# Optimization experiments

Hardware: AMD Instinct MI355X
Metric: run time of the kernel (lower is better)

Reference implementation:

```python
import jax, jax.numpy as jnp
import numpy as np

N = 8192      # nodes
D_IN = 128    # input features
D_H = 48      # GAT hidden (hardcoded in module)
D_OUT = 32    # control output dim
NEG_INF = -9e15  # matches torch code's -9000000000000000.0


def setup_inputs() -> dict:
    key = jax.random.key(0)
    ks = jax.random.split(key, 12)
    s = 0.05
    return {
        "x": jax.random.normal(ks[0], (N, D_IN), jnp.float32),
        "adj": jax.random.randint(ks[1], (N, N), 0, 2, jnp.int32),
        "W_gat": jax.random.normal(ks[2], (D_H, D_IN), jnp.float32) * s,
        "a": jax.random.normal(ks[3], (1, D_H), jnp.float32) * s,
        "gamma": jnp.ones((D_H,), jnp.float32),
        "beta": jnp.zeros((D_H,), jnp.float32),
        "W1": jax.random.normal(ks[4], (256, D_H), jnp.float32) * s,
        "b1": jnp.zeros((256,), jnp.float32),
        "W2": jax.random.normal(ks[5], (128, 256), jnp.float32) * s,
        "b2": jnp.zeros((128,), jnp.float32),
        "W3": jax.random.normal(ks[6], (D_OUT, 128), jnp.float32) * s,
        "b3": jnp.zeros((D_OUT,), jnp.float32),
    }


def reference(x, adj, W_gat, a, gamma, beta, W1, b1, W2, b2, W3, b3):
    # --- LightweightGATLayer ---
    Wh = x @ W_gat.T                      # [N, D_H]
    s = Wh @ a.T                          # [N, 1] additive attention scores
    e = s + s.T                           # [N, N]
    e = jnp.where(e > 0, e, 0.2 * e)      # LeakyReLU(0.2)
    e = jnp.where(adj > 0, e, NEG_INF)    # mask non-edges
    attn = jax.nn.softmax(e, axis=1)      # row softmax; dropout is identity in eval
    h_prime = attn @ Wh                   # [N, D_H]
    # LayerNorm over last dim, eps=1e-5
    mu = jnp.mean(h_prime, axis=-1, keepdims=True)
    var = jnp.var(h_prime, axis=-1, keepdims=True)
    h = (h_prime - mu) * jax.lax.rsqrt(var + 1e-5) * gamma + beta
    # --- BiACT MLP head: 48 -> 256 -> 128 -> D_OUT ---
    h = jax.nn.relu(h @ W1.T + b1)
    h = jax.nn.relu(h @ W2.T + b2)
    return h @ W3.T + b3                  # [N, D_OUT]
```

## Files before the change

### kernel.cpp

```cpp
#include <hip/hip_runtime.h>

#define N 8192
#define DIN 128
#define DH 48
#define MT 256
#define KC 64
#define PSTR (KC + 8)
#define NSPLIT 16
#define JSPAN (N / NSPLIT)
#define NCHUNK (JSPAN / KC)
#define ACC_STRIDE 64
#define RB 32

typedef _Float16 half8 __attribute__((ext_vector_type(8)));
typedef float f32x4 __attribute__((ext_vector_type(4)));

__global__ __launch_bounds__(256) void k_wh(const float* __restrict__ x,
                                            const float* __restrict__ Wg,
                                            float* __restrict__ Wh) {
    __shared__ float wT[DIN * DH];
    int t = threadIdx.x;
    for (int e = t; e < DIN * DH; e += 256) {
        int c = e / DIN, k = e % DIN;
        wT[k * DH + c] = Wg[e];
    }
    __syncthreads();
    int o = blockIdx.x * 256 + t;
    int r = o / DH, c = o % DH;
    const float4* xr = (const float4*)(x + (size_t)r * DIN);
    float acc = 0.f;
    #pragma unroll 8
    for (int k4 = 0; k4 < DIN / 4; ++k4) {
        float4 xv = xr[k4];
        int kb = k4 * 4;
        acc += xv.x * wT[(kb + 0) * DH + c];
        acc += xv.y * wT[(kb + 1) * DH + c];
        acc += xv.z * wT[(kb + 2) * DH + c];
        acc += xv.w * wT[(kb + 3) * DH + c];
    }
    Wh[o] = acc;
}

__global__ __launch_bounds__(256) void k_s(const float* __restrict__ Wh,
                                           const float* __restrict__ a,
                                           float* __restrict__ s) {
    int r = blockIdx.x * 256 + threadIdx.x;
    const float4* wr = (const float4*)(Wh + (size_t)r * DH);
    const float4* av = (const float4*)a;
    float acc = 0.f;
    #pragma unroll
    for (int k4 = 0; k4 < DH / 4; ++k4) {
        float4 w = wr[k4]; float4 aa = av[k4];
        acc += w.x * aa.x + w.y * aa.y + w.z * aa.z + w.w * aa.w;
    }
    s[r] = acc;
}

__global__ __launch_bounds__(256) void k_gat(const int* __restrict__ adj,
                                             const float* __restrict__ Wh,
                                             const float* __restrict__ s,
                                             float* __restrict__ accWs) {
    __shared__ _Float16 pS[MT][PSTR];
    __shared__ _Float16 wS[64][PSTR];
    __shared__ float sRow[MT];
    int t = threadIdx.x;
    int tile = blockIdx.x & 31;
    int split = blockIdx.x >> 5;
    int i0 = tile * MT;
    int jbase = split * JSPAN;

    sRow[t] = s[i0 + t];
    for (int e = t; e < 16 * PSTR; e += 256) {
        int n = 48 + e / PSTR, k = e % PSTR;
        wS[n][k] = (n == 48) ? (_Float16)1.0f : (_Float16)0.0f;
    }

    int lane = t & 63, w = t >> 6;
    int ln16 = lane & 15, kq = lane >> 4;
    int jp = t & 31, rg = t >> 5;

    f32x4 acc[4][4];
    #pragma unroll
    for (int a0 = 0; a0 < 4; ++a0)
        #pragma unroll
        for (int b0 = 0; b0 < 4; ++b0) acc[a0][b0] = (f32x4){0.f, 0.f, 0.f, 0.f};

    __syncthreads();

    for (int chunk = 0; chunk < NCHUNK; ++chunk) {
        int j0 = jbase + chunk * KC;
        #pragma unroll
        for (int k = 0; k < 12; ++k) {
            int e = t + k * 256;
            int jc = e / DH, d = e % DH;
            wS[d][jc] = (_Float16)Wh[(size_t)j0 * DH + e];
        }
        {
            float2 sj = *(const float2*)(s + j0 + 2 * jp);
            #pragma unroll 8
            for (int it = 0; it < 32; ++it) {
                int r = rg * 32 + it;
                int2 av = *(const int2*)(adj + (size_t)(i0 + r) * N + j0 + 2 * jp);
                float e0 = sRow[r] + sj.x;
                float e1 = sRow[r] + sj.y;
                e0 = fmaxf(e0, 0.2f * e0);
                e1 = fmaxf(e1, 0.2f * e1);
                float p0 = av.x ? __expf(e0) : 0.f;
                float p1 = av.y ? __expf(e1) : 0.f;
                union { _Float16 h[2]; unsigned u; } pk;
                pk.h[0] = (_Float16)p0;
                pk.h[1] = (_Float16)p1;
                *(unsigned*)&pS[r][2 * jp] = pk.u;
            }
        }
        __syncthreads();
        {
            const int m0 = w * 64;
            #pragma unroll
            for (int kt = 0; kt < 2; ++kt) {
                const int kk = kt * 32 + kq * 8;
                half8 b[4];
                #pragma unroll
                for (int nt = 0; nt < 4; ++nt)
                    b[nt] = *(const half8*)&wS[nt * 16 + ln16][kk];
                #pragma unroll
                for (int mtl = 0; mtl < 4; ++mtl) {
                    half8 a = *(const half8*)&pS[m0 + mtl * 16 + ln16][kk];
                    #pragma unroll
                    for (int nt = 0; nt < 4; ++nt)
                        acc[mtl][nt] = __builtin_amdgcn_mfma_f32_16x16x32_f16(
                            a, b[nt], acc[mtl][nt], 0, 0, 0);
                }
            }
        }
        __syncthreads();
    }
    size_t rbase = (size_t)split * N + i0;
    #pragma unroll
    for (int mtl = 0; mtl < 4; ++mtl) {
        #pragma unroll
        for (int nt = 0; nt < 4; ++nt) {
            int col = nt * 16 + ln16;
            if (nt == 3 && ln16 != 0) continue;
            #pragma unroll
            for (int reg = 0; reg < 4; ++reg) {
                int row = w * 64 + mtl * 16 + kq * 4 + reg;
                accWs[(rbase + row) * ACC_STRIDE + col] = acc[mtl][nt][reg];
            }
        }
    }
}

__global__ __launch_bounds__(256) void k_mlp(const float* __restrict__ accWs,
                                             const float* __restrict__ gamma,
                                             const float* __restrict__ beta,
                                             const float* __restrict__ W1, const float* __restrict__ b1,
                                             const float* __restrict__ W2, const float* __restrict__ b2,
                                             const float* __restrict__ W3, const float* __restrict__ b3,
                                             float* __restrict__ out) {
    __shared__ float hacc[RB * 49];
    __shared__ float hN[RB * DH];
    __shared__ float h1[RB * 256];
    __shared__ float h2[RB * 128];
    int t = threadIdx.x;
    int r0 = blockIdx.x * RB;

    for (int e = t; e < RB * 49; e += 256) {
        int r = e / 49, d = e % 49;
        size_t base = (size_t)(r0 + r) * ACC_STRIDE + d;
        float v = 0.f;
        #pragma unroll
        for (int sp = 0; sp < NSPLIT; ++sp)
            v += accWs[(size_t)sp * N * ACC_STRIDE + base];
        hacc[r * 49 + d] = v;
    }
    __syncthreads();

    if (t < RB) {
        float invl = 1.f / hacc[t * 49 + 48];
        float sum = 0.f;
        for (int d = 0; d < DH; ++d) sum += hacc[t * 49 + d];
        float mean = sum * invl * (1.f / DH);
        float var = 0.f;
        for (int d = 0; d < DH; ++d) {
            float dv = hacc[t * 49 + d] * invl - mean;
            var += dv * dv;
        }
        var *= (1.f / DH);
        float rs = rsqrtf(var + 1e-5f);
        for (int d = 0; d < DH; ++d) {
            float hv = (hacc[t * 49 + d] * invl - mean) * rs;
            hN[t * DH + d] = hv * gamma[d] + beta[d];
        }
    }
    __syncthreads();

    {
        int c = t;
        float4 wreg[12];
        const float4* wrow = (const float4*)(W1 + c * DH);
        #pragma unroll
        for (int k4 = 0; k4 < 12; ++k4) wreg[k4] = wrow[k4];
        float bias = b1[c];
        for (int r = 0; r < RB; ++r) {
            float acc = bias;
            const float4* hv4 = (const float4*)&hN[r * DH];
            #pragma unroll
            for (int k4 = 0; k4 < 12; ++k4) {
                float4 hv = hv4[k4];
                acc += hv.x * wreg[k4].x + hv.y * wreg[k4].y
                     + hv.z * wreg[k4].z + hv.w * wreg[k4].w;
            }
            h1[r * 256 + c] = fmaxf(acc, 0.f);
        }
    }
    __syncthreads();

    {
        int c = t & 127;
        int g = t >> 7;
        int rb = g * 16;
        float acc[16];
        float bias = b2[c];
        #pragma unroll
        for (int r = 0; r < 16; ++r) acc[r] = bias;
        const float4* wrow = (const float4*)(W2 + c * 256);
        for (int k4 = 0; k4 < 64; ++k4) {
            float4 wv = wrow[k4];
            #pragma unroll
            for (int r = 0; r < 16; ++r) {
                const float4 hv = *(const float4*)(&h1[(rb + r) * 256 + k4 * 4]);
                acc[r] += wv.x * hv.x + wv.y * hv.y + wv.z * hv.z + wv.w * hv.w;
            }
        }
        #pragma unroll
        for (int r = 0; r < 16; ++r)
            h2[(rb + r) * 128 + c] = fmaxf(acc[r], 0.f);
    }
    __syncthreads();

    {
        int c = t & 31;
        int g = t >> 5;
        int rb = g * 4;
        float acc[4];
        float bias = b3[c];
        #pragma unroll
        for (int r = 0; r < 4; ++r) acc[r] = bias;
        const float4* wrow = (const float4*)(W3 + c * 128);
        for (int k4 = 0; k4 < 32; ++k4) {
            float4 wv = wrow[k4];
            #pragma unroll
            for (int r = 0; r < 4; ++r) {
                const float4 hv = *(const float4*)(&h2[(rb + r) * 128 + k4 * 4]);
                acc[r] += wv.x * hv.x + wv.y * hv.y + wv.z * hv.z + wv.w * hv.w;
            }
        }
        #pragma unroll
        for (int r = 0; r < 4; ++r)
            out[(size_t)(r0 + rb + r) * 32 + c] = acc[r];
    }
}

extern "C" void kernel_launch(void* const* d_in, const int* in_sizes, int n_in,
                              void* d_out, int out_size, void* d_ws, size_t ws_size,
                              hipStream_t stream) {
    const float* x     = (const float*)d_in[0];
    const int*   adj   = (const int*)d_in[1];
    const float* Wg    = (const float*)d_in[2];
    const float* a     = (const float*)d_in[3];
    const float* gamma = (const float*)d_in[4];
    const float* beta  = (const float*)d_in[5];
    const float* W1    = (const float*)d_in[6];
    const float* b1    = (const float*)d_in[7];
    const float* W2    = (const float*)d_in[8];
    const float* b2    = (const float*)d_in[9];
    const float* W3    = (const float*)d_in[10];
    const float* b3    = (const float*)d_in[11];
    float* out = (float*)d_out;

    float* ws = (float*)d_ws;
    float* Wh    = ws;
    float* s     = ws + (size_t)N * DH;
    float* accWs = s + N;

    k_wh<<<N * DH / 256, 256, 0, stream>>>(x, Wg, Wh);
    k_s<<<N / 256, 256, 0, stream>>>(Wh, a, s);
    k_gat<<<32 * NSPLIT, 256, 0, stream>>>(adj, Wh, s, accWs);
    k_mlp<<<N / RB, 256, 0, stream>>>(accWs, gamma, beta, W1, b1, W2, b2, W3, b3, out);
}
```

Baseline: 463.4 us.

## Halve GAT tile, pre-transpose Wh to fp16, atomically reduce splits, retile MLP

The GAT row tile shrinks from 256 to 128 rows, which doubles the grid, and the kernel sets launch bounds for higher occupancy. Wh is pre-transposed to fp16 in a separate kernel so B fragments load straight from global memory instead of being staged through LDS. The denominator column now comes from a constant register fragment, and the adjacency loads for a chunk are batched up front. The 16 split partials are combined with atomicAdd into a zeroed buffer rather than written out and summed in the MLP. The MLP layers 1 and 2 are also retiled for more register reuse. In exchange this adds extra launches, atomic traffic and re-reads of adjacency-independent data per tile.

```diff
diff --git a/kernel.cpp b/kernel.cpp
--- a/kernel.cpp
+++ b/kernel.cpp
@@ -3,17 +3,22 @@
 #define N 8192
 #define DIN 128
 #define DH 48
-#define MT 256
+#define MT 128
 #define KC 64
-#define PSTR (KC + 8)
+#define PSTR 72
 #define NSPLIT 16
 #define JSPAN (N / NSPLIT)
 #define NCHUNK (JSPAN / KC)
-#define ACC_STRIDE 64
+#define HSTR 49
 #define RB 32
 
 typedef _Float16 half8 __attribute__((ext_vector_type(8)));
 typedef float f32x4 __attribute__((ext_vector_type(4)));
+
+__global__ __launch_bounds__(256) void k_zero(float* __restrict__ hacc) {
+    int i = blockIdx.x * 256 + threadIdx.x;
+    if (i < N * HSTR) hacc[i] = 0.f;
+}
 
 __global__ __launch_bounds__(256) void k_wh(const float* __restrict__ x,
                                             const float* __restrict__ Wg,
@@ -56,57 +61,82 @@
     s[r] = acc;
 }
 
-__global__ __launch_bounds__(256) void k_gat(const int* __restrict__ adj,
-                                             const float* __restrict__ Wh,
-                                             const float* __restrict__ s,
-                                             float* __restrict__ accWs) {
+__global__ __launch_bounds__(256) void k_tr(const float* __restrict__ Wh,
+                                            _Float16* __restrict__ WhT) {
+    __shared__ _Float16 tile[DH][72];
+    int t = threadIdx.x;
+    int r0 = blockIdx.x * 64;
+    for (int e = t; e < 64 * DH; e += 256) {
+        int r = e / DH, c = e % DH;
+        tile[c][r] = (_Float16)Wh[(size_t)(r0 + r) * DH + c];
+    }
+    __syncthreads();
+    for (int u = t; u < DH * 8; u += 256) {
+        int c = u >> 3, g = u & 7;
+        *(half8*)&WhT[(size_t)c * N + r0 + g * 8] = *(const half8*)&tile[c][g * 8];
+    }
+}
+
+__global__ __launch_bounds__(256, 4) void k_gat(const int* __restrict__ adj,
+                                                const _Float16* __restrict__ WhT,
+                                                const float* __restrict__ s,
+                                                float* __restrict__ hacc) {
     __shared__ _Float16 pS[MT][PSTR];
-    __shared__ _Float16 wS[64][PSTR];
     __shared__ float sRow[MT];
     int t = threadIdx.x;
-    int tile = blockIdx.x & 31;
-    int split = blockIdx.x >> 5;
+    int tile = blockIdx.x & 63;
+    int split = blockIdx.x >> 6;
     int i0 = tile * MT;
     int jbase = split * JSPAN;
 
-    sRow[t] = s[i0 + t];
-    for (int e = t; e < 16 * PSTR; e += 256) {
-        int n = 48 + e / PSTR, k = e % PSTR;
-        wS[n][k] = (n == 48) ? (_Float16)1.0f : (_Float16)0.0f;
-    }
+    if (t < MT) sRow[t] = s[i0 + t];
 
     int lane = t & 63, w = t >> 6;
     int ln16 = lane & 15, kq = lane >> 4;
     int jp = t & 31, rg = t >> 5;
 
-    f32x4 acc[4][4];
+    half8 bc;
+    {
+        _Float16 v = (ln16 == 0) ? (_Float16)1.0f : (_Float16)0.0f;
+        #pragma unroll
+        for (int i = 0; i < 8; ++i) bc[i] = v;
+    }
+
+    f32x4 acc[2][4];
     #pragma unroll
-    for (int a0 = 0; a0 < 4; ++a0)
-        #pragma unroll
-        for (int b0 = 0; b0 < 4; ++b0) acc[a0][b0] = (f32x4){0.f, 0.f, 0.f, 0.f};
+    for (int m = 0; m < 2; ++m)
+        #pragma unroll
+        for (int n = 0; n < 4; ++n) acc[m][n] = (f32x4){0.f, 0.f, 0.f, 0.f};
 
     __syncthreads();
 
     for (int chunk = 0; chunk < NCHUNK; ++chunk) {
         int j0 = jbase + chunk * KC;
-        #pragma unroll
-        for (int k = 0; k < 12; ++k) {
-            int e = t + k * 256;
-            int jc = e / DH, d = e % DH;
-            wS[d][jc] = (_Float16)Wh[(size_t)j0 * DH + e];
-        }
+        int2 av[16];
+        {
+            const int* abase = adj + (size_t)(i0 + rg * 16) * N + j0 + 2 * jp;
+            #pragma unroll
+            for (int it = 0; it < 16; ++it)
+                av[it] = *(const int2*)(abase + (size_t)it * N);
+        }
+        half8 bfr[2][3];
+        #pragma unroll
+        for (int kt = 0; kt < 2; ++kt)
+            #pragma unroll
+            for (int nt = 0; nt < 3; ++nt)
+                bfr[kt][nt] = *(const half8*)&WhT[(size_t)(nt * 16 + ln16) * N
+                                                  + j0 + kt * 32 + kq * 8];
         {
             float2 sj = *(const float2*)(s + j0 + 2 * jp);
-            #pragma unroll 8
-            for (int it = 0; it < 32; ++it) {
-                int r = rg * 32 + it;
-                int2 av = *(const int2*)(adj + (size_t)(i0 + r) * N + j0 + 2 * jp);
+            #pragma unroll
+            for (int it = 0; it < 16; ++it) {
+                int r = rg * 16 + it;
                 float e0 = sRow[r] + sj.x;
                 float e1 = sRow[r] + sj.y;
                 e0 = fmaxf(e0, 0.2f * e0);
                 e1 = fmaxf(e1, 0.2f * e1);
-                float p0 = av.x ? __expf(e0) : 0.f;
-                float p1 = av.y ? __expf(e1) : 0.f;
+                float p0 = av[it].x ? __expf(e0) : 0.f;
+                float p1 = av[it].y ? __expf(e1) : 0.f;
                 union { _Float16 h[2]; unsigned u; } pk;
                 pk.h[0] = (_Float16)p0;
                 pk.h[1] = (_Float16)p1;
@@ -115,150 +145,147 @@
         }
         __syncthreads();
         {
-            const int m0 = w * 64;
+            int m0 = w * 32;
             #pragma unroll
             for (int kt = 0; kt < 2; ++kt) {
-                const int kk = kt * 32 + kq * 8;
-                half8 b[4];
+                int kk = kt * 32 + kq * 8;
                 #pragma unroll
-                for (int nt = 0; nt < 4; ++nt)
-                    b[nt] = *(const half8*)&wS[nt * 16 + ln16][kk];
-                #pragma unroll
-                for (int mtl = 0; mtl < 4; ++mtl) {
+                for (int mtl = 0; mtl < 2; ++mtl) {
                     half8 a = *(const half8*)&pS[m0 + mtl * 16 + ln16][kk];
-                    #pragma unroll
-                    for (int nt = 0; nt < 4; ++nt)
-                        acc[mtl][nt] = __builtin_amdgcn_mfma_f32_16x16x32_f16(
-                            a, b[nt], acc[mtl][nt], 0, 0, 0);
+                    acc[mtl][0] = __builtin_amdgcn_mfma_f32_16x16x32_f16(a, bfr[kt][0], acc[mtl][0], 0, 0, 0);
+                    acc[mtl][1] = __builtin_amdgcn_mfma_f32_16x16x32_f16(a, bfr[kt][1], acc[mtl][1], 0, 0, 0);
+                    acc[mtl][2] = __builtin_amdgcn_mfma_f32_16x16x32_f16(a, bfr[kt][2], acc[mtl][2], 0, 0, 0);
+                    acc[mtl][3] = __builtin_amdgcn_mfma_f32_16x16x32_f16(a, bc,         acc[mtl][3], 0, 0, 0);
                 }
             }
         }
         __syncthreads();
     }
-    size_t rbase = (size_t)split * N + i0;
     #pragma unroll
-    for (int mtl = 0; mtl < 4; ++mtl) {
+    for (int mtl = 0; mtl < 2; ++mtl) {
+        int rbase = i0 + w * 32 + mtl * 16 + kq * 4;
         #pragma unroll
         for (int nt = 0; nt < 4; ++nt) {
             int col = nt * 16 + ln16;
             if (nt == 3 && ln16 != 0) continue;
             #pragma unroll
-            for (int reg = 0; reg < 4; ++reg) {
-                int row = w * 64 + mtl * 16 + kq * 4 + reg;
-                accWs[(rbase + row) * ACC_STRIDE + col] = acc[mtl][nt][reg];
-            }
-        }
-    }
-}
-
-__global__ __launch_bounds__(256) void k_mlp(const float* __restrict__ accWs,
+            for (int reg = 0; reg < 4; ++reg)
+                atomicAdd(&hacc[(size_t)(rbase + reg) * HSTR + col], acc[mtl][nt][reg]);
+        }
+    }
+}
+
+__global__ __launch_bounds__(256) void k_mlp(const float* __restrict__ hacc,
                                              const float* __restrict__ gamma,
                                              const float* __restrict__ beta,
                                              const float* __restrict__ W1, const float* __restrict__ b1,
                                              const float* __restrict__ W2, const float* __restrict__ b2,
                                              const float* __restrict__ W3, const float* __restrict__ b3,
                                              float* __restrict__ out) {
-    __shared__ float hacc[RB * 49];
+    __shared__ float hs[RB * HSTR];
     __shared__ float hN[RB * DH];
     __shared__ float h1[RB * 256];
     __shared__ float h2[RB * 128];
     int t = threadIdx.x;
     int r0 = blockIdx.x * RB;
 
-    for (int e = t; e < RB * 49; e += 256) {
-        int r = e / 49, d = e % 49;
-        size_t base = (size_t)(r0 + r) * ACC_STRIDE + d;
-        float v = 0.f;
-        #pragma unroll
-        for (int sp = 0; sp < NSPLIT; ++sp)
-            v += accWs[(size_t)sp * N * ACC_STRIDE + base];
-        hacc[r * 49 + d] = v;
-    }
+    for (int e = t; e < RB * HSTR; e += 256)
+        hs[e] = hacc[(size_t)r0 * HSTR + e];
     __syncthreads();
 
     if (t < RB) {
-        float invl = 1.f / hacc[t * 49 + 48];
+        float invl = 1.f / hs[t * HSTR + 48];
         float sum = 0.f;
-        for (int d = 0; d < DH; ++d) sum += hacc[t * 49 + d];
+        for (int d = 0; d < DH; ++d) sum += hs[t * HSTR + d];
         float mean = sum * invl * (1.f / DH);
         float var = 0.f;
         for (int d = 0; d < DH; ++d) {
-            float dv = hacc[t * 49 + d] * invl - mean;
+            float dv = hs[t * HSTR + d] * invl - mean;
             var += dv * dv;
         }
         var *= (1.f / DH);
         float rs = rsqrtf(var + 1e-5f);
         for (int d = 0; d < DH; ++d) {
-            float hv = (hacc[t * 49 + d] * invl - mean) * rs;
+            float hv = (hs[t * HSTR + d] * invl - mean) * rs;
             hN[t * DH + d] = hv * gamma[d] + beta[d];
         }
     }
     __syncthreads();
 
     {
-        int c = t;
-        float4 wreg[12];
-        const float4* wrow = (const float4*)(W1 + c * DH);
-        #pragma unroll
-        for (int k4 = 0; k4 < 12; ++k4) wreg[k4] = wrow[k4];
-        float bias = b1[c];
-        for (int r = 0; r < RB; ++r) {
-            float acc = bias;
+        int c0 = (t & 127) * 2, c1 = c0 + 1;
+        int rbeg = (t >> 7) * 16;
+        float4 wa[12], wb[12];
+        const float4* wr0 = (const float4*)(W1 + c0 * DH);
+        const float4* wr1 = (const float4*)(W1 + c1 * DH);
+        #pragma unroll
+        for (int k4 = 0; k4 < 12; ++k4) { wa[k4] = wr0[k4]; wb[k4] = wr1[k4]; }
+        float ba = b1[c0], bb = b1[c1];
+        for (int r = rbeg; r < rbeg + 16; ++r) {
             const float4* hv4 = (const float4*)&hN[r * DH];
+            float a0 = ba, a1 = bb;
             #pragma unroll
             for (int k4 = 0; k4 < 12; ++k4) {
                 float4 hv = hv4[k4];
-                acc += hv.x * wreg[k4].x + hv.y * wreg[k4].y
-                     + hv.z * wreg[k4].z + hv.w * wreg[k4].w;
+                a0 += hv.x * wa[k4].x + hv.y * wa[k4].y + hv.z * wa[k4].z + hv.w * wa[k4].w;
+                a1 += hv.x * wb[k4].x + hv.y * wb[k4].y + hv.z * wb[k4].z + hv.w * wb[k4].w;
             }
-            h1[r * 256 + c] = fmaxf(acc, 0.f);
+            h1[r * 256 + c0] = fmaxf(a0, 0.f);
+            h1[r * 256 + c1] = fmaxf(a1, 0.f);
         }
     }
     __syncthreads();
 
     {
-        int c = t & 127;
-        int g = t >> 7;
-        int rb = g * 16;
-        float acc[16];
-        float bias = b2[c];
-        #pragma unroll
-        for (int r = 0; r < 16; ++r) acc[r] = bias;
-        const float4* wrow = (const float4*)(W2 + c * 256);
+        int c4 = (t & 31) * 4;
+        int rr0 = (t >> 5) * 4;
+        float a[4][4];
+        #pragma unroll
+        for (int rr = 0; rr < 4; ++rr)
+            #pragma unroll
+            for (int cc = 0; cc < 4; ++cc) a[rr][cc] = 0.f;
         for (int k4 = 0; k4 < 64; ++k4) {
-            float4 wv = wrow[k4];
-            #pragma unroll
-            for (int r = 0; r < 16; ++r) {
-                const float4 hv = *(const float4*)(&h1[(rb + r) * 256 + k4 * 4]);
-                acc[r] += wv.x * hv.x + wv.y * hv.y + wv.z * hv.z + wv.w * hv.w;
-            }
-        }
-        #pragma unroll
-        for (int r = 0; r < 16; ++r)
-            h2[(rb + r) * 128 + c] = fmaxf(acc[r], 0.f);
+            float4 h[4], wv[4];
+            #pragma unroll
+            for (int rr = 0; rr < 4; ++rr)
+                h[rr] = *(const float4*)&h1[(rr0 + rr) * 256 + 4 * k4];
+            #pragma unroll
+            for (int cc = 0; cc < 4; ++cc)
+                wv[cc] = *(const float4*)&W2[(size_t)(c4 + cc) * 256 + 4 * k4];
+            #pragma unroll
+            for (int rr = 0; rr < 4; ++rr)
+                #pragma unroll
+                for (int cc = 0; cc < 4; ++cc)
+                    a[rr][cc] += h[rr].x * wv[cc].x + h[rr].y * wv[cc].y
+                               + h[rr].z * wv[cc].z + h[rr].w * wv[cc].w;
+        }
+        #pragma unroll
+        for (int rr = 0; rr < 4; ++rr)
+            #pragma unroll
+            for (int cc = 0; cc < 4; ++cc)
+                h2[(rr0 + rr) * 128 + c4 + cc] = fmaxf(a[rr][cc] + b2[c4 + cc], 0.f);
     }
     __syncthreads();
 
     {
         int c = t & 31;
-        int g = t >> 5;
-        int rb = g * 4;
-        float acc[4];
+        int rr0 = (t >> 5) * 4;
+        float a[4];
         float bias = b3[c];
         #pragma unroll
-        for (int r = 0; r < 4; ++r) acc[r] = bias;
+        for (int rr = 0; rr < 4; ++rr) a[rr] = bias;
         const float4* wrow = (const float4*)(W3 + c * 128);
         for (int k4 = 0; k4 < 32; ++k4) {
             float4 wv = wrow[k4];
             #pragma unroll
-            for (int r = 0; r < 4; ++r) {
-                const float4 hv = *(const float4*)(&h2[(rb + r) * 128 + k4 * 4]);
-                acc[r] += wv.x * hv.x + wv.y * hv.y + wv.z * hv.z + wv.w * hv.w;
+            for (int rr = 0; rr < 4; ++rr) {
+                float4 hv = *(const float4*)&h2[(rr0 + rr) * 128 + 4 * k4];
+                a[rr] += wv.x * hv.x + wv.y * hv.y + wv.z * hv.z + wv.w * hv.w;
             }
         }
         #pragma unroll
-        for (int r = 0; r < 4; ++r)
-            out[(size_t)(r0 + rb + r) * 32 + c] = acc[r];
+        for (int rr = 0; rr < 4; ++rr)
+            out[(size_t)(r0 + rr0 + rr) * 32 + c] = a[rr];
     }
 }
 
@@ -280,12 +307,15 @@
     float* out = (float*)d_out;
 
     float* ws = (float*)d_ws;
-    float* Wh    = ws;
-    float* s     = ws + (size_t)N * DH;
-    float* accWs = s + N;
-
+    float*     Wh   = ws;
+    float*     s    = ws + (size_t)N * DH;
+    _Float16*  WhT  = (_Float16*)(ws + (size_t)N * DH + N);
+    float*     hacc = ws + (size_t)N * DH + N + (size_t)N * DH / 2;
+
+    k_zero<<<(N * HSTR + 255) / 256, 256, 0, stream>>>(hacc);
     k_wh<<<N * DH / 256, 256, 0, stream>>>(x, Wg, Wh);
     k_s<<<N / 256, 256, 0, stream>>>(Wh, a, s);
-    k_gat<<<32 * NSPLIT, 256, 0, stream>>>(adj, Wh, s, accWs);
-    k_mlp<<<N / RB, 256, 0, stream>>>(accWs, gamma, beta, W1, b1, W2, b2, W3, b3, out);
-}
+    k_tr<<<N / 64, 256, 0, stream>>>(Wh, WhT);
+    k_gat<<<64 * NSPLIT, 256, 0, stream>>>(adj, WhT, s, hacc);
+    k_mlp<<<N / RB, 256, 0, stream>>>(hacc, gamma, beta, W1, b1, W2, b2, W3, b3, out);
+}
```

Result: slower. 497.6 us (+7.4%).
